# Kernel optimization log

Measured on AMD Instinct MI355X. Metric: run time of the kernel, lower is better.

Reference implementation:

```python
import jax, jax.numpy as jnp
import numpy as np

D, H, WIN, OUT = 3, 64, 8, 32
B, T = 128, 129
IU, JU = np.triu_indices(D, k=1)  # Lyndon pairs i<j at depth 2


def setup_inputs() -> dict:
    key = jax.random.key(0)
    ks = jax.random.split(key, 10)
    ts = jnp.broadcast_to(jnp.linspace(0.0, 1.0, T), (B, T))
    # path-like control values: cumulative sum of small increments
    x = jnp.cumsum(0.1 * jax.random.normal(ks[0], (B, T, D)), axis=1)
    def lin(k, o, i):
        return jax.random.normal(k, (o, i), dtype=jnp.float32) * (1.0 / np.sqrt(i))
    return {
        "ts": ts, "x": x,
        "W0": lin(ks[1], 128, D), "b0": jnp.zeros((128,), jnp.float32),
        "W1": lin(ks[2], 128, 128), "b1": jnp.zeros((128,), jnp.float32),
        "W2": lin(ks[3], H, 128), "b2": jnp.zeros((H,), jnp.float32),
        "V0": lin(ks[4], 128, H), "c0": jnp.zeros((128,), jnp.float32),
        "V1": lin(ks[5], 128, 128), "c1": jnp.zeros((128,), jnp.float32),
        "V2": lin(ks[6], D * H, 128), "c2": jnp.zeros((D * H,), jnp.float32),
        "R": lin(ks[7], OUT, H), "rb": jnp.zeros((OUT,), jnp.float32),
    }


def reference(ts, x, W0, b0, W1, b1, W2, b2, V0, c0, V1, c1, V2, c2, R, rb):
    sp = jax.nn.softplus

    def init_mlp(v):  # R^D -> R^H, Euclidean retract = identity
        return W2 @ sp(W1 @ sp(W0 @ v + b0) + b1) + b2

    def vf_flat(y):  # R^H -> R^{D*H}, final tanh (split_multi_vector_field)
        return jnp.tanh(V2 @ sp(V1 @ sp(V0 @ y + c0) + c1) + c2)

    def F(y):
        # level-1 fields f_i(y) as rows of m: (D, H)
        m = vf_flat(y).reshape(D, H)
        # J[a, b] = D f_b(y) . f_a(y)  via JVPs in directions f_a
        J = jax.vmap(lambda v: jax.jvp(vf_flat, (y,), (v,))[1].reshape(D, H))(m)
        # Lyndon level-2 brackets [f_i, f_j] = Df_j.f_i - Df_i.f_j
        br = J[IU, JU] - J[JU, IU]  # (D*(D-1)/2, H)
        return jnp.concatenate([m, br], axis=0).T  # (H, logsig_size)

    def logsigs_fn(xs):  # depth-2 log-signatures over disjoint windows
        nw = (T - 1) // WIN
        idx = (np.arange(nw) * WIN)[:, None] + np.arange(WIN + 1)[None, :]
        win = xs[idx]
        lvl1 = win[:, -1] - win[:, 0]       # increments
        rel = win[:, :-1] - win[:, :1]      # path relative to window start
        dv = win[:, 1:] - win[:, :-1]       # increments within window
        a = jnp.einsum('nki,nkj->nij', rel, dv)
        area = 0.5 * (a - jnp.swapaxes(a, 1, 2))  # Levy areas
        return jnp.concatenate([lvl1, area[:, IU, JU]], axis=1)

    def solve_one(t, xs):
        h0 = init_mlp(xs[0])
        ls = logsigs_fn(xs)                       # (nw, L)
        t_sig = t[::WIN]                          # window knot times
        slopes = ls / (t_sig[1:] - t_sig[:-1])[:, None]  # dz/dt per window
        slope_steps = jnp.repeat(slopes, WIN, axis=0)    # (T-1, L)
        dts = t[1:] - t[:-1]

        def step(y, inp):  # Heun integration of dy = F(y) dz/dt dt
            dt, s = inp
            k1 = F(y) @ s
            k2 = F(y + dt * k1) @ s
            yn = y + 0.5 * dt * (k1 + k2)
            return yn, yn

        _, ys = jax.lax.scan(step, h0, (dts, slope_steps))
        hidden = jnp.concatenate([h0[None], ys], axis=0)  # (T, H)
        return jnp.tanh(hidden @ R.T + rb)                # evolving readout

    return jax.vmap(solve_one)(ts, x)  # (B, T, OUT)
```

## Files before the change

### kernel.cpp

```cpp
#include <hip/hip_runtime.h>
#include <math.h>

#define BB 128
#define TT 129
#define NSTEP 128
#define NW 16
#define WINW 8
#define OUTD 32

typedef _Float16 h2_t __attribute__((ext_vector_type(2)));

__device__ __forceinline__ float fast_rcp(float v){ return __builtin_amdgcn_rcpf(v); }
__device__ __forceinline__ float softplus_f(float v){ return fmaxf(v,0.f)+__logf(1.f+__expf(-fabsf(v))); }
__device__ __forceinline__ float sigmoid_f(float v){ return fast_rcp(1.f+__expf(-v)); }
__device__ __forceinline__ float tanh_f(float v){
    float ax=fminf(fabsf(v),15.f); float e=__expf(2.f*ax);
    float r=1.f-2.f*fast_rcp(e+1.f); return copysignf(r,v);
}
__device__ __forceinline__ float pack2(float a,float b){
    h2_t h; h.x=(_Float16)a; h.y=(_Float16)b; return __builtin_bit_cast(float,h);
}
__device__ __forceinline__ float dot2c(float wc,float ac,float acc){
    return __builtin_amdgcn_fdot2(__builtin_bit_cast(h2_t,wc),__builtin_bit_cast(h2_t,ac),acc,false);
}
__device__ __forceinline__ float dot2q(float4 wq,float4 aq,float acc){
    acc=dot2c(wq.x,aq.x,acc); acc=dot2c(wq.y,aq.y,acc);
    acc=dot2c(wq.z,aq.z,acc); acc=dot2c(wq.w,aq.w,acc); return acc;
}
#define DOT4(acc,Wv,Av) acc += (Wv).x*(Av).x + (Wv).y*(Av).y + (Wv).z*(Av).z + (Wv).w*(Av).w
#define PIN4(v) asm volatile("" : "+v"((v).x), "+v"((v).y), "+v"((v).z), "+v"((v).w))

#define DPPF(x,ctrl) __builtin_bit_cast(float, __builtin_amdgcn_update_dpp(0, __builtin_bit_cast(int,(x)), (ctrl), 0xF, 0xF, true))
__device__ __forceinline__ float dpp_xor1(float x){ return DPPF(x,0xB1); }
__device__ __forceinline__ float dpp_xor2(float x){ return DPPF(x,0x4E); }
__device__ __forceinline__ float dpp_hmir(float x){ return DPPF(x,0x141); }

__global__ __launch_bounds__(256, 1)
void ncde_solve(const float* __restrict__ ts, const float* __restrict__ x,
                const float* __restrict__ W0, const float* __restrict__ b0,
                const float* __restrict__ W1, const float* __restrict__ b1,
                const float* __restrict__ W2, const float* __restrict__ b2,
                const float* __restrict__ V0, const float* __restrict__ c0,
                const float* __restrict__ V1, const float* __restrict__ c1,
                const float* __restrict__ V2, const float* __restrict__ c2,
                const float* __restrict__ R, const float* __restrict__ rb,
                float* __restrict__ out)
{
    const int b = blockIdx.x;
    const int tid = threadIdx.x;
    const int r = tid >> 2, q = tid & 3;
    const int prow = tid >> 3, poct = tid & 7;

    __shared__ __align__(16) float RSh[OUTD*68];
    __shared__ __align__(16) float ySh[64];
    __shared__ __align__(16) float yp[32], y2p[32];
    __shared__ __align__(16) float a0H[64], a1H[64];
    __shared__ __align__(16) float mpH[96];
    __shared__ __align__(16) float u0H[192], u1H[192];
    __shared__ float slopesSh[NW][6];
    __shared__ float dtsSh[NSTEP];

    float4 v0c[2][2], v1c[2][4], v2c[3][4];
    {
        auto pkld = [](const float* src)->float4{
            const float4* p=(const float4*)src;
            float4 a=p[0], c=p[1];
            float4 rr; rr.x=pack2(a.x,a.y); rr.y=pack2(a.z,a.w); rr.z=pack2(c.x,c.y); rr.w=pack2(c.z,c.w);
            return rr;
        };
        #pragma unroll
        for (int i=0;i<2;i++){
            const float* base = V0 + (r+64*i)*64 + q*16;
            v0c[i][0]=pkld(base); v0c[i][1]=pkld(base+8);
        }
        #pragma unroll
        for (int i=0;i<2;i++){
            const float* base = V1 + (r+64*i)*128 + q*32;
            #pragma unroll
            for (int k=0;k<4;k++) v1c[i][k]=pkld(base+8*k);
        }
        #pragma unroll
        for (int i=0;i<3;i++){
            const float* base = V2 + (r+64*i)*128 + q*32;
            #pragma unroll
            for (int k=0;k<4;k++) v2c[i][k]=pkld(base+8*k);
        }
        #pragma unroll
        for (int i=0;i<2;i++){ PIN4(v0c[i][0]); PIN4(v0c[i][1]); }
        #pragma unroll
        for (int i=0;i<2;i++){
            #pragma unroll
            for (int k=0;k<4;k++) PIN4(v1c[i][k]);
        }
        #pragma unroll
        for (int i=0;i<3;i++){
            #pragma unroll
            for (int k=0;k<4;k++) PIN4(v2c[i][k]);
        }
    }
    const float c0A=c0[r], c0B=c0[64+r];
    const float c1A=c1[r], c1B=c1[64+r];
    const float c2A=c2[r], c2B=c2[64+r], c2C=c2[128+r];
    const float rbp = rb[prow];

    for (int i=tid; i<OUTD*64; i+=256) RSh[(i>>6)*68 + (i&63)] = R[i];
    const float* tsb = ts + b*TT;
    for (int i=tid; i<NSTEP; i+=256) dtsSh[i] = tsb[i+1] - tsb[i];

    if (tid < NW) {
        const int w = tid;
        const float* xs = x + (size_t)(b*TT + w*WINW)*3;
        float x0c[3] = {xs[0], xs[1], xs[2]};
        float prev[3] = {x0c[0], x0c[1], x0c[2]};
        float am01=0.f, am02=0.f, am12=0.f, am10=0.f, am20=0.f, am21=0.f;
        #pragma unroll
        for (int k=0;k<WINW;k++) {
            float cur[3] = {xs[(k+1)*3+0], xs[(k+1)*3+1], xs[(k+1)*3+2]};
            float rel[3], dv[3];
            #pragma unroll
            for (int c=0;c<3;c++){ rel[c]=prev[c]-x0c[c]; dv[c]=cur[c]-prev[c]; }
            am01 += rel[0]*dv[1]; am10 += rel[1]*dv[0];
            am02 += rel[0]*dv[2]; am20 += rel[2]*dv[0];
            am12 += rel[1]*dv[2]; am21 += rel[2]*dv[1];
            prev[0]=cur[0]; prev[1]=cur[1]; prev[2]=cur[2];
        }
        const float invden = 1.f/(tsb[(w+1)*WINW] - tsb[w*WINW]);
        slopesSh[w][0] = (prev[0]-x0c[0])*invden;
        slopesSh[w][1] = (prev[1]-x0c[1])*invden;
        slopesSh[w][2] = (prev[2]-x0c[2])*invden;
        slopesSh[w][3] = 0.5f*(am01-am10)*invden;
        slopesSh[w][4] = 0.5f*(am02-am20)*invden;
        slopesSh[w][5] = 0.5f*(am12-am21)*invden;
    }

    if (tid < 128) {
        const float xv0 = x[(size_t)b*TT*3+0];
        const float xv1 = x[(size_t)b*TT*3+1];
        const float xv2 = x[(size_t)b*TT*3+2];
        float acc = b0[tid] + W0[tid*3]*xv0 + W0[tid*3+1]*xv1 + W0[tid*3+2]*xv2;
        u0H[tid] = softplus_f(acc);
    }
    __syncthreads();
    if (tid < 128) {
        float acc = b1[tid];
        const float4* rw = (const float4*)(W1 + tid*128);
        #pragma unroll 8
        for (int k=0;k<32;k++){ float4 wv=rw[k]; float4 av=*(const float4*)&u0H[4*k]; DOT4(acc,wv,av); }
        u1H[tid] = softplus_f(acc);
    }
    __syncthreads();
    if (tid < 64) {
        float acc = b2[tid];
        const float4* rw = (const float4*)(W2 + tid*128);
        #pragma unroll 8
        for (int k=0;k<32;k++){ float4 wv=rw[k]; float4 av=*(const float4*)&u1H[4*k]; DOT4(acc,wv,av); }
        ySh[tid] = acc;
        ((_Float16*)yp)[tid] = (_Float16)acc;
    }
    __syncthreads();

    float yreg = ySh[r];
    float k1r = 0.f;
    float S0,S1,S2,S3,S4,S5;

    auto Feval = [&](const float* ypIn, bool first, float dtc) {
        float sig0A,sig0B,sig1A,sig1B,mA,mB,mC,dtA,dtB,dtC;
        {
            const float4* Y = (const float4*)ypIn + q*2;
            float4 y0=Y[0], y1=Y[1];
            float zA=0.f, zB=0.f;
            zA=dot2q(v0c[0][0],y0,zA); zA=dot2q(v0c[0][1],y1,zA);
            zB=dot2q(v0c[1][0],y0,zB); zB=dot2q(v0c[1][1],y1,zB);
            zA += dpp_xor1(zA); zA += dpp_xor2(zA); zA += c0A;
            zB += dpp_xor1(zB); zB += dpp_xor2(zB); zB += c0B;
            sig0A=sigmoid_f(zA); sig0B=sigmoid_f(zB);
            if (!q){
                ((_Float16*)a0H)[r]    = (_Float16)softplus_f(zA);
                ((_Float16*)a0H)[64+r] = (_Float16)softplus_f(zB);
            }
        }
        __syncthreads();
        {
            const float4* A = (const float4*)a0H + q*4;
            float4 a0=A[0],a1=A[1],a2=A[2],a3=A[3];
            float zA=0.f, zB=0.f;
            zA=dot2q(v1c[0][0],a0,zA); zA=dot2q(v1c[0][1],a1,zA); zA=dot2q(v1c[0][2],a2,zA); zA=dot2q(v1c[0][3],a3,zA);
            zB=dot2q(v1c[1][0],a0,zB); zB=dot2q(v1c[1][1],a1,zB); zB=dot2q(v1c[1][2],a2,zB); zB=dot2q(v1c[1][3],a3,zB);
            zA += dpp_xor1(zA); zA += dpp_xor2(zA); zA += c1A;
            zB += dpp_xor1(zB); zB += dpp_xor2(zB); zB += c1B;
            sig1A=sigmoid_f(zA); sig1B=sigmoid_f(zB);
            if (!q){
                ((_Float16*)a1H)[r]    = (_Float16)softplus_f(zA);
                ((_Float16*)a1H)[64+r] = (_Float16)softplus_f(zB);
            }
        }
        __syncthreads();
        {
            const float4* A = (const float4*)a1H + q*4;
            float4 a0=A[0],a1=A[1],a2=A[2],a3=A[3];
            float zA=0.f, zB=0.f, zC=0.f;
            zA=dot2q(v2c[0][0],a0,zA); zA=dot2q(v2c[0][1],a1,zA); zA=dot2q(v2c[0][2],a2,zA); zA=dot2q(v2c[0][3],a3,zA);
            zB=dot2q(v2c[1][0],a0,zB); zB=dot2q(v2c[1][1],a1,zB); zB=dot2q(v2c[1][2],a2,zB); zB=dot2q(v2c[1][3],a3,zB);
            zC=dot2q(v2c[2][0],a0,zC); zC=dot2q(v2c[2][1],a1,zC); zC=dot2q(v2c[2][2],a2,zC); zC=dot2q(v2c[2][3],a3,zC);
            zA += dpp_xor1(zA); zA += dpp_xor2(zA);
            zB += dpp_xor1(zB); zB += dpp_xor2(zB);
            zC += dpp_xor1(zC); zC += dpp_xor2(zC);
            mA=tanh_f(zA+c2A); mB=tanh_f(zB+c2B); mC=tanh_f(zC+c2C);
            dtA=1.f-mA*mA; dtB=1.f-mB*mB; dtC=1.f-mC*mC;
            if (!q){
                ((_Float16*)mpH)[r]     = (_Float16)mA;
                ((_Float16*)mpH)[64+r]  = (_Float16)mB;
                ((_Float16*)mpH)[128+r] = (_Float16)mC;
            }
        }
        __syncthreads();
        {
            const float4* M = (const float4*)mpH;
            float4 g00=M[q*2], g01=M[q*2+1];
            float4 g10=M[8+q*2], g11=M[8+q*2+1];
            float4 g20=M[16+q*2], g21=M[16+q*2+1];
            float t0A=0.f,t1A=0.f,t2A=0.f,t0B=0.f,t1B=0.f,t2B=0.f;
            t0A=dot2q(v0c[0][0],g00,t0A); t0A=dot2q(v0c[0][1],g01,t0A);
            t1A=dot2q(v0c[0][0],g10,t1A); t1A=dot2q(v0c[0][1],g11,t1A);
            t2A=dot2q(v0c[0][0],g20,t2A); t2A=dot2q(v0c[0][1],g21,t2A);
            t0B=dot2q(v0c[1][0],g00,t0B); t0B=dot2q(v0c[1][1],g01,t0B);
            t1B=dot2q(v0c[1][0],g10,t1B); t1B=dot2q(v0c[1][1],g11,t1B);
            t2B=dot2q(v0c[1][0],g20,t2B); t2B=dot2q(v0c[1][1],g21,t2B);
            t0A += dpp_xor1(t0A); t0A += dpp_xor2(t0A);
            t1A += dpp_xor1(t1A); t1A += dpp_xor2(t1A);
            t2A += dpp_xor1(t2A); t2A += dpp_xor2(t2A);
            t0B += dpp_xor1(t0B); t0B += dpp_xor2(t0B);
            t1B += dpp_xor1(t1B); t1B += dpp_xor2(t1B);
            t2B += dpp_xor1(t2B); t2B += dpp_xor2(t2B);
            if (!q){
                ((_Float16*)u0H)[r]      = (_Float16)(sig0A*t0A);
                ((_Float16*)u0H)[64+r]   = (_Float16)(sig0B*t0B);
                ((_Float16*)u0H)[128+r]  = (_Float16)(sig0A*t1A);
                ((_Float16*)u0H)[192+r]  = (_Float16)(sig0B*t1B);
                ((_Float16*)u0H)[256+r]  = (_Float16)(sig0A*t2A);
                ((_Float16*)u0H)[320+r]  = (_Float16)(sig0B*t2B);
            }
        }
        __syncthreads();
        {
            const float4* U = (const float4*)u0H;
            float4 g0[4],g1[4],g2[4];
            #pragma unroll
            for (int k=0;k<4;k++){ g0[k]=U[q*4+k]; g1[k]=U[16+q*4+k]; g2[k]=U[32+q*4+k]; }
            float t0A=0.f,t1A=0.f,t2A=0.f,t0B=0.f,t1B=0.f,t2B=0.f;
            #pragma unroll
            for (int k=0;k<4;k++){
                float4 wa=v1c[0][k], wb=v1c[1][k];
                t0A=dot2q(wa,g0[k],t0A); t1A=dot2q(wa,g1[k],t1A); t2A=dot2q(wa,g2[k],t2A);
                t0B=dot2q(wb,g0[k],t0B); t1B=dot2q(wb,g1[k],t1B); t2B=dot2q(wb,g2[k],t2B);
            }
            t0A += dpp_xor1(t0A); t0A += dpp_xor2(t0A);
            t1A += dpp_xor1(t1A); t1A += dpp_xor2(t1A);
            t2A += dpp_xor1(t2A); t2A += dpp_xor2(t2A);
            t0B += dpp_xor1(t0B); t0B += dpp_xor2(t0B);
            t1B += dpp_xor1(t1B); t1B += dpp_xor2(t1B);
            t2B += dpp_xor1(t2B); t2B += dpp_xor2(t2B);
            if (!q){
                ((_Float16*)u1H)[r]      = (_Float16)(sig1A*t0A);
                ((_Float16*)u1H)[64+r]   = (_Float16)(sig1B*t0B);
                ((_Float16*)u1H)[128+r]  = (_Float16)(sig1A*t1A);
                ((_Float16*)u1H)[192+r]  = (_Float16)(sig1B*t1B);
                ((_Float16*)u1H)[256+r]  = (_Float16)(sig1A*t2A);
                ((_Float16*)u1H)[320+r]  = (_Float16)(sig1B*t2B);
            }
        }
        __syncthreads();
        {
            const float4* U = (const float4*)u1H;
            float4 g0[4],g1[4],g2[4];
            #pragma unroll
            for (int k=0;k<4;k++){ g0[k]=U[q*4+k]; g1[k]=U[16+q*4+k]; g2[k]=U[32+q*4+k]; }
            float J1r=0.f,J2r=0.f,J0m=0.f,J2m=0.f,J0t=0.f,J1t=0.f;
            #pragma unroll
            for (int k=0;k<4;k++){
                float4 wa=v2c[0][k], wb=v2c[1][k], wc=v2c[2][k];
                J1r=dot2q(wa,g1[k],J1r); J2r=dot2q(wa,g2[k],J2r);
                J0m=dot2q(wb,g0[k],J0m); J2m=dot2q(wb,g2[k],J2m);
                J0t=dot2q(wc,g0[k],J0t); J1t=dot2q(wc,g1[k],J1t);
            }
            J1r += dpp_xor1(J1r); J1r += dpp_xor2(J1r);
            J2r += dpp_xor1(J2r); J2r += dpp_xor2(J2r);
            J0m += dpp_xor1(J0m); J0m += dpp_xor2(J0m);
            J2m += dpp_xor1(J2m); J2m += dpp_xor2(J2m);
            J0t += dpp_xor1(J0t); J0t += dpp_xor2(J0t);
            J1t += dpp_xor1(J1t); J1t += dpp_xor2(J1t);
            J1r*=dtA; J2r*=dtA; J0m*=dtB; J2m*=dtB; J0t*=dtC; J1t*=dtC;
            float kk = mA*S0 + mB*S1 + mC*S2
                     + S3*(J0m - J1r) + S4*(J0t - J2r) + S5*(J1t - J2m);
            if (first){
                k1r = kk;
                float y2 = yreg + dtc*kk;
                if (!q) ((_Float16*)y2p)[r] = (_Float16)y2;
            } else {
                yreg += 0.5f*dtc*(k1r + kk);
                if (!q){ ((_Float16*)yp)[r] = (_Float16)yreg; ySh[r] = yreg; }
            }
        }
        __syncthreads();
    };

    auto proj = [&](int stp) {
        const float4* rr = (const float4*)(RSh + prow*68 + poct*8);
        const float4* yy = (const float4*)(ySh + poct*8);
        float pacc = 0.f;
        DOT4(pacc, rr[0], yy[0]); DOT4(pacc, rr[1], yy[1]);
        pacc += dpp_xor1(pacc);
        pacc += dpp_xor2(pacc);
        pacc += dpp_hmir(pacc);
        if (!poct) out[(size_t)(b*TT + stp)*OUTD + prow] = tanh_f(pacc + rbp);
    };

    for (int step=0; step<NSTEP; ++step) {
        proj(step);
        const int w = step >> 3;
        S0=slopesSh[w][0]; S1=slopesSh[w][1]; S2=slopesSh[w][2];
        S3=slopesSh[w][3]; S4=slopesSh[w][4]; S5=slopesSh[w][5];
        const float dtc = dtsSh[step];
        Feval(yp,  true,  dtc);
        Feval(y2p, false, dtc);
    }
    proj(NSTEP);
}

extern "C" void kernel_launch(void* const* d_in, const int* in_sizes, int n_in,
                              void* d_out, int out_size, void* d_ws, size_t ws_size,
                              hipStream_t stream) {
    const float* ts = (const float*)d_in[0];
    const float* x  = (const float*)d_in[1];
    const float* W0 = (const float*)d_in[2];
    const float* b0 = (const float*)d_in[3];
    const float* W1 = (const float*)d_in[4];
    const float* b1 = (const float*)d_in[5];
    const float* W2 = (const float*)d_in[6];
    const float* b2 = (const float*)d_in[7];
    const float* V0 = (const float*)d_in[8];
    const float* c0 = (const float*)d_in[9];
    const float* V1 = (const float*)d_in[10];
    const float* c1 = (const float*)d_in[11];
    const float* V2 = (const float*)d_in[12];
    const float* c2 = (const float*)d_in[13];
    const float* R  = (const float*)d_in[14];
    const float* rb = (const float*)d_in[15];
    float* out = (float*)d_out;

    ncde_solve<<<dim3(BB), dim3(256), 0, stream>>>(
        ts, x, W0, b0, W1, b1, W2, b2, V0, c0, V1, c1, V2, c2, R, rb, out);
}
```

Measured before the change: 617.2 us.

## Pack two batch elements per 512-thread block with shared barriers

Each block now handles two batch elements. Two 256-thread halves index their own per-element shared buffers and share RSh and the __syncthreads barriers. This halves the grid from 128 to 64 blocks on a GPU with many more CUs. The intent is to interleave two independent serial chains inside one CU to hide latency, but it uses fewer CUs, the shared barriers couple both halves, and register pressure per CU goes up.

New measurement: 870.4 us. +41.0%, slower.

```diff
diff --git a/kernel.cpp b/kernel.cpp
--- a/kernel.cpp
+++ b/kernel.cpp
@@ -7,6 +7,7 @@
 #define NW 16
 #define WINW 8
 #define OUTD 32
+#define NB 2
 
 typedef _Float16 h2_t __attribute__((ext_vector_type(2)));
 
@@ -35,7 +36,7 @@
 __device__ __forceinline__ float dpp_xor2(float x){ return DPPF(x,0x4E); }
 __device__ __forceinline__ float dpp_hmir(float x){ return DPPF(x,0x141); }
 
-__global__ __launch_bounds__(256, 1)
+__global__ __launch_bounds__(512, 1)
 void ncde_solve(const float* __restrict__ ts, const float* __restrict__ x,
                 const float* __restrict__ W0, const float* __restrict__ b0,
                 const float* __restrict__ W1, const float* __restrict__ b1,
@@ -46,19 +47,21 @@
                 const float* __restrict__ R, const float* __restrict__ rb,
                 float* __restrict__ out)
 {
-    const int b = blockIdx.x;
     const int tid = threadIdx.x;
-    const int r = tid >> 2, q = tid & 3;
-    const int prow = tid >> 3, poct = tid & 7;
+    const int u = tid >> 8;
+    const int t = tid & 255;
+    const int b = blockIdx.x * NB + u;
+    const int r = t >> 2, q = t & 3;
+    const int prow = t >> 3, poct = t & 7;
 
     __shared__ __align__(16) float RSh[OUTD*68];
-    __shared__ __align__(16) float ySh[64];
-    __shared__ __align__(16) float yp[32], y2p[32];
-    __shared__ __align__(16) float a0H[64], a1H[64];
-    __shared__ __align__(16) float mpH[96];
-    __shared__ __align__(16) float u0H[192], u1H[192];
-    __shared__ float slopesSh[NW][6];
-    __shared__ float dtsSh[NSTEP];
+    __shared__ __align__(16) float ySh[NB][64];
+    __shared__ __align__(16) float yp[NB][32], y2p[NB][32];
+    __shared__ __align__(16) float a0H[NB][64], a1H[NB][64];
+    __shared__ __align__(16) float mpH[NB][96];
+    __shared__ __align__(16) float u0H[NB][192], u1H[NB][192];
+    __shared__ float slopesSh[NB][NW][6];
+    __shared__ float dtsSh[NB][NSTEP];
 
     float4 v0c[2][2], v1c[2][4], v2c[3][4];
     {
@@ -103,12 +106,12 @@
     const float c2A=c2[r], c2B=c2[64+r], c2C=c2[128+r];
     const float rbp = rb[prow];
 
-    for (int i=tid; i<OUTD*64; i+=256) RSh[(i>>6)*68 + (i&63)] = R[i];
-    const float* tsb = ts + b*TT;
-    for (int i=tid; i<NSTEP; i+=256) dtsSh[i] = tsb[i+1] - tsb[i];
-
-    if (tid < NW) {
-        const int w = tid;
+    for (int i=tid; i<OUTD*64; i+=512) RSh[(i>>6)*68 + (i&63)] = R[i];
+    const float* tsb = ts + (size_t)b*TT;
+    for (int i=t; i<NSTEP; i+=256) dtsSh[u][i] = tsb[i+1] - tsb[i];
+
+    if (t < NW) {
+        const int w = t;
         const float* xs = x + (size_t)(b*TT + w*WINW)*3;
         float x0c[3] = {xs[0], xs[1], xs[2]};
         float prev[3] = {x0c[0], x0c[1], x0c[2]};
@@ -125,41 +128,41 @@
             prev[0]=cur[0]; prev[1]=cur[1]; prev[2]=cur[2];
         }
         const float invden = 1.f/(tsb[(w+1)*WINW] - tsb[w*WINW]);
-        slopesSh[w][0] = (prev[0]-x0c[0])*invden;
-        slopesSh[w][1] = (prev[1]-x0c[1])*invden;
-        slopesSh[w][2] = (prev[2]-x0c[2])*invden;
-        slopesSh[w][3] = 0.5f*(am01-am10)*invden;
-        slopesSh[w][4] = 0.5f*(am02-am20)*invden;
-        slopesSh[w][5] = 0.5f*(am12-am21)*invden;
-    }
-
-    if (tid < 128) {
+        slopesSh[u][w][0] = (prev[0]-x0c[0])*invden;
+        slopesSh[u][w][1] = (prev[1]-x0c[1])*invden;
+        slopesSh[u][w][2] = (prev[2]-x0c[2])*invden;
+        slopesSh[u][w][3] = 0.5f*(am01-am10)*invden;
+        slopesSh[u][w][4] = 0.5f*(am02-am20)*invden;
+        slopesSh[u][w][5] = 0.5f*(am12-am21)*invden;
+    }
+
+    if (t < 128) {
         const float xv0 = x[(size_t)b*TT*3+0];
         const float xv1 = x[(size_t)b*TT*3+1];
         const float xv2 = x[(size_t)b*TT*3+2];
-        float acc = b0[tid] + W0[tid*3]*xv0 + W0[tid*3+1]*xv1 + W0[tid*3+2]*xv2;
-        u0H[tid] = softplus_f(acc);
+        float acc = b0[t] + W0[t*3]*xv0 + W0[t*3+1]*xv1 + W0[t*3+2]*xv2;
+        u0H[u][t] = softplus_f(acc);
     }
     __syncthreads();
-    if (tid < 128) {
-        float acc = b1[tid];
-        const float4* rw = (const float4*)(W1 + tid*128);
+    if (t < 128) {
+        float acc = b1[t];
+        const float4* rw = (const float4*)(W1 + t*128);
         #pragma unroll 8
-        for (int k=0;k<32;k++){ float4 wv=rw[k]; float4 av=*(const float4*)&u0H[4*k]; DOT4(acc,wv,av); }
-        u1H[tid] = softplus_f(acc);
+        for (int k=0;k<32;k++){ float4 wv=rw[k]; float4 av=*(const float4*)&u0H[u][4*k]; DOT4(acc,wv,av); }
+        u1H[u][t] = softplus_f(acc);
     }
     __syncthreads();
-    if (tid < 64) {
-        float acc = b2[tid];
-        const float4* rw = (const float4*)(W2 + tid*128);
+    if (t < 64) {
+        float acc = b2[t];
+        const float4* rw = (const float4*)(W2 + t*128);
         #pragma unroll 8
-        for (int k=0;k<32;k++){ float4 wv=rw[k]; float4 av=*(const float4*)&u1H[4*k]; DOT4(acc,wv,av); }
-        ySh[tid] = acc;
-        ((_Float16*)yp)[tid] = (_Float16)acc;
+        for (int k=0;k<32;k++){ float4 wv=rw[k]; float4 av=*(const float4*)&u1H[u][4*k]; DOT4(acc,wv,av); }
+        ySh[u][t] = acc;
+        ((_Float16*)yp[u])[t] = (_Float16)acc;
     }
     __syncthreads();
 
-    float yreg = ySh[r];
+    float yreg = ySh[u][r];
     float k1r = 0.f;
     float S0,S1,S2,S3,S4,S5;
 
@@ -175,13 +178,13 @@
             zB += dpp_xor1(zB); zB += dpp_xor2(zB); zB += c0B;
             sig0A=sigmoid_f(zA); sig0B=sigmoid_f(zB);
             if (!q){
-                ((_Float16*)a0H)[r]    = (_Float16)softplus_f(zA);
-                ((_Float16*)a0H)[64+r] = (_Float16)softplus_f(zB);
-            }
-        }
-        __syncthreads();
-        {
-            const float4* A = (const float4*)a0H + q*4;
+                ((_Float16*)a0H[u])[r]    = (_Float16)softplus_f(zA);
+                ((_Float16*)a0H[u])[64+r] = (_Float16)softplus_f(zB);
+            }
+        }
+        __syncthreads();
+        {
+            const float4* A = (const float4*)a0H[u] + q*4;
             float4 a0=A[0],a1=A[1],a2=A[2],a3=A[3];
             float zA=0.f, zB=0.f;
             zA=dot2q(v1c[0][0],a0,zA); zA=dot2q(v1c[0][1],a1,zA); zA=dot2q(v1c[0][2],a2,zA); zA=dot2q(v1c[0][3],a3,zA);
@@ -190,13 +193,13 @@
             zB += dpp_xor1(zB); zB += dpp_xor2(zB); zB += c1B;
             sig1A=sigmoid_f(zA); sig1B=sigmoid_f(zB);
             if (!q){
-                ((_Float16*)a1H)[r]    = (_Float16)softplus_f(zA);
-                ((_Float16*)a1H)[64+r] = (_Float16)softplus_f(zB);
-            }
-        }
-        __syncthreads();
-        {
-            const float4* A = (const float4*)a1H + q*4;
+                ((_Float16*)a1H[u])[r]    = (_Float16)softplus_f(zA);
+                ((_Float16*)a1H[u])[64+r] = (_Float16)softplus_f(zB);
+            }
+        }
+        __syncthreads();
+        {
+            const float4* A = (const float4*)a1H[u] + q*4;
             float4 a0=A[0],a1=A[1],a2=A[2],a3=A[3];
             float zA=0.f, zB=0.f, zC=0.f;
             zA=dot2q(v2c[0][0],a0,zA); zA=dot2q(v2c[0][1],a1,zA); zA=dot2q(v2c[0][2],a2,zA); zA=dot2q(v2c[0][3],a3,zA);
@@ -208,14 +211,14 @@
             mA=tanh_f(zA+c2A); mB=tanh_f(zB+c2B); mC=tanh_f(zC+c2C);
             dtA=1.f-mA*mA; dtB=1.f-mB*mB; dtC=1.f-mC*mC;
             if (!q){
-                ((_Float16*)mpH)[r]     = (_Float16)mA;
-                ((_Float16*)mpH)[64+r]  = (_Float16)mB;
-                ((_Float16*)mpH)[128+r] = (_Float16)mC;
-            }
-        }
-        __syncthreads();
-        {
-            const float4* M = (const float4*)mpH;
+                ((_Float16*)mpH[u])[r]     = (_Float16)mA;
+                ((_Float16*)mpH[u])[64+r]  = (_Float16)mB;
+                ((_Float16*)mpH[u])[128+r] = (_Float16)mC;
+            }
+        }
+        __syncthreads();
+        {
+            const float4* M = (const float4*)mpH[u];
             float4 g00=M[q*2], g01=M[q*2+1];
             float4 g10=M[8+q*2], g11=M[8+q*2+1];
             float4 g20=M[16+q*2], g21=M[16+q*2+1];
@@ -233,17 +236,17 @@
             t1B += dpp_xor1(t1B); t1B += dpp_xor2(t1B);
             t2B += dpp_xor1(t2B); t2B += dpp_xor2(t2B);
             if (!q){
-                ((_Float16*)u0H)[r]      = (_Float16)(sig0A*t0A);
-                ((_Float16*)u0H)[64+r]   = (_Float16)(sig0B*t0B);
-                ((_Float16*)u0H)[128+r]  = (_Float16)(sig0A*t1A);
-                ((_Float16*)u0H)[192+r]  = (_Float16)(sig0B*t1B);
-                ((_Float16*)u0H)[256+r]  = (_Float16)(sig0A*t2A);
-                ((_Float16*)u0H)[320+r]  = (_Float16)(sig0B*t2B);
-            }
-        }
-        __syncthreads();
-        {
-            const float4* U = (const float4*)u0H;
+                ((_Float16*)u0H[u])[r]      = (_Float16)(sig0A*t0A);
+                ((_Float16*)u0H[u])[64+r]   = (_Float16)(sig0B*t0B);
+                ((_Float16*)u0H[u])[128+r]  = (_Float16)(sig0A*t1A);
+                ((_Float16*)u0H[u])[192+r]  = (_Float16)(sig0B*t1B);
+                ((_Float16*)u0H[u])[256+r]  = (_Float16)(sig0A*t2A);
+                ((_Float16*)u0H[u])[320+r]  = (_Float16)(sig0B*t2B);
+            }
+        }
+        __syncthreads();
+        {
+            const float4* U = (const float4*)u0H[u];
             float4 g0[4],g1[4],g2[4];
             #pragma unroll
             for (int k=0;k<4;k++){ g0[k]=U[q*4+k]; g1[k]=U[16+q*4+k]; g2[k]=U[32+q*4+k]; }
@@ -261,17 +264,17 @@
             t1B += dpp_xor1(t1B); t1B += dpp_xor2(t1B);
             t2B += dpp_xor1(t2B); t2B += dpp_xor2(t2B);
             if (!q){
-                ((_Float16*)u1H)[r]      = (_Float16)(sig1A*t0A);
-                ((_Float16*)u1H)[64+r]   = (_Float16)(sig1B*t0B);
-                ((_Float16*)u1H)[128+r]  = (_Float16)(sig1A*t1A);
-                ((_Float16*)u1H)[192+r]  = (_Float16)(sig1B*t1B);
-                ((_Float16*)u1H)[256+r]  = (_Float16)(sig1A*t2A);
-                ((_Float16*)u1H)[320+r]  = (_Float16)(sig1B*t2B);
-            }
-        }
-        __syncthreads();
-        {
-            const float4* U = (const float4*)u1H;
+                ((_Float16*)u1H[u])[r]      = (_Float16)(sig1A*t0A);
+                ((_Float16*)u1H[u])[64+r]   = (_Float16)(sig1B*t0B);
+                ((_Float16*)u1H[u])[128+r]  = (_Float16)(sig1A*t1A);
+                ((_Float16*)u1H[u])[192+r]  = (_Float16)(sig1B*t1B);
+                ((_Float16*)u1H[u])[256+r]  = (_Float16)(sig1A*t2A);
+                ((_Float16*)u1H[u])[320+r]  = (_Float16)(sig1B*t2B);
+            }
+        }
+        __syncthreads();
+        {
+            const float4* U = (const float4*)u1H[u];
             float4 g0[4],g1[4],g2[4];
             #pragma unroll
             for (int k=0;k<4;k++){ g0[k]=U[q*4+k]; g1[k]=U[16+q*4+k]; g2[k]=U[32+q*4+k]; }
@@ -295,10 +298,10 @@
             if (first){
                 k1r = kk;
                 float y2 = yreg + dtc*kk;
-                if (!q) ((_Float16*)y2p)[r] = (_Float16)y2;
+                if (!q) ((_Float16*)y2p[u])[r] = (_Float16)y2;
             } else {
                 yreg += 0.5f*dtc*(k1r + kk);
-                if (!q){ ((_Float16*)yp)[r] = (_Float16)yreg; ySh[r] = yreg; }
+                if (!q){ ((_Float16*)yp[u])[r] = (_Float16)yreg; ySh[u][r] = yreg; }
             }
         }
         __syncthreads();
@@ -306,7 +309,7 @@
 
     auto proj = [&](int stp) {
         const float4* rr = (const float4*)(RSh + prow*68 + poct*8);
-        const float4* yy = (const float4*)(ySh + poct*8);
+        const float4* yy = (const float4*)(ySh[u] + poct*8);
         float pacc = 0.f;
         DOT4(pacc, rr[0], yy[0]); DOT4(pacc, rr[1], yy[1]);
         pacc += dpp_xor1(pacc);
@@ -318,11 +321,11 @@
     for (int step=0; step<NSTEP; ++step) {
         proj(step);
         const int w = step >> 3;
-        S0=slopesSh[w][0]; S1=slopesSh[w][1]; S2=slopesSh[w][2];
-        S3=slopesSh[w][3]; S4=slopesSh[w][4]; S5=slopesSh[w][5];
-        const float dtc = dtsSh[step];
-        Feval(yp,  true,  dtc);
-        Feval(y2p, false, dtc);
+        S0=slopesSh[u][w][0]; S1=slopesSh[u][w][1]; S2=slopesSh[u][w][2];
+        S3=slopesSh[u][w][3]; S4=slopesSh[u][w][4]; S5=slopesSh[u][w][5];
+        const float dtc = dtsSh[u][step];
+        Feval(yp[u],  true,  dtc);
+        Feval(y2p[u], false, dtc);
     }
     proj(NSTEP);
 }
@@ -348,6 +351,6 @@
     const float* rb = (const float*)d_in[15];
     float* out = (float*)d_out;
 
-    ncde_solve<<<dim3(BB), dim3(256), 0, stream>>>(
+    ncde_solve<<<dim3(BB/NB), dim3(512), 0, stream>>>(
         ts, x, W0, b0, W1, b1, W2, b2, V0, c0, V1, c1, V2, c2, R, rb, out);
 }
```

## Split each row's dot products across eight lanes with 512-thread blocks

Applied to the files above, without the earlier changes.

Doubles the block size to 512 threads and assigns each output row to 8 lanes instead of 4. Each lane now keeps half as many packed fp16 weights in registers and performs half as many dot2 ops per stage, with a three-step DPP reduction replacing the two-step one. The intent is to shorten the serial per-step critical path of the latency-bound Heun loop. The cost is more waves taking part in every barrier and one extra cross-lane reduction step per dot product.

New measurement: 692.0 us. 12.1% more time.

```diff
diff --git a/kernel.cpp b/kernel.cpp
--- a/kernel.cpp
+++ b/kernel.cpp
@@ -34,8 +34,9 @@
 __device__ __forceinline__ float dpp_xor1(float x){ return DPPF(x,0xB1); }
 __device__ __forceinline__ float dpp_xor2(float x){ return DPPF(x,0x4E); }
 __device__ __forceinline__ float dpp_hmir(float x){ return DPPF(x,0x141); }
-
-__global__ __launch_bounds__(256, 1)
+#define RED8(x) do{ x += dpp_xor1(x); x += dpp_xor2(x); x += dpp_hmir(x); }while(0)
+
+__global__ __launch_bounds__(512, 1)
 void ncde_solve(const float* __restrict__ ts, const float* __restrict__ x,
                 const float* __restrict__ W0, const float* __restrict__ b0,
                 const float* __restrict__ W1, const float* __restrict__ b1,
@@ -47,9 +48,9 @@
                 float* __restrict__ out)
 {
     const int b = blockIdx.x;
-    const int tid = threadIdx.x;
-    const int r = tid >> 2, q = tid & 3;
-    const int prow = tid >> 3, poct = tid & 7;
+    const int t = threadIdx.x;
+    const int r = t >> 3, q = t & 7;
+    const int prow = t >> 3, poct = t & 7;
 
     __shared__ __align__(16) float RSh[OUTD*68];
     __shared__ __align__(16) float ySh[64];
@@ -60,7 +61,7 @@
     __shared__ float slopesSh[NW][6];
     __shared__ float dtsSh[NSTEP];
 
-    float4 v0c[2][2], v1c[2][4], v2c[3][4];
+    float4 v0c[2], v1c[2][2], v2c[3][2];
     {
         auto pkld = [](const float* src)->float4{
             const float4* p=(const float4*)src;
@@ -69,46 +70,35 @@
             return rr;
         };
         #pragma unroll
+        for (int i=0;i<2;i++) v0c[i]=pkld(V0 + (r+64*i)*64 + q*8);
+        #pragma unroll
         for (int i=0;i<2;i++){
-            const float* base = V0 + (r+64*i)*64 + q*16;
-            v0c[i][0]=pkld(base); v0c[i][1]=pkld(base+8);
-        }
-        #pragma unroll
-        for (int i=0;i<2;i++){
-            const float* base = V1 + (r+64*i)*128 + q*32;
-            #pragma unroll
-            for (int k=0;k<4;k++) v1c[i][k]=pkld(base+8*k);
+            const float* base = V1 + (r+64*i)*128 + q*16;
+            v1c[i][0]=pkld(base); v1c[i][1]=pkld(base+8);
         }
         #pragma unroll
         for (int i=0;i<3;i++){
-            const float* base = V2 + (r+64*i)*128 + q*32;
-            #pragma unroll
-            for (int k=0;k<4;k++) v2c[i][k]=pkld(base+8*k);
-        }
-        #pragma unroll
-        for (int i=0;i<2;i++){ PIN4(v0c[i][0]); PIN4(v0c[i][1]); }
-        #pragma unroll
-        for (int i=0;i<2;i++){
-            #pragma unroll
-            for (int k=0;k<4;k++) PIN4(v1c[i][k]);
-        }
-        #pragma unroll
-        for (int i=0;i<3;i++){
-            #pragma unroll
-            for (int k=0;k<4;k++) PIN4(v2c[i][k]);
-        }
+            const float* base = V2 + (r+64*i)*128 + q*16;
+            v2c[i][0]=pkld(base); v2c[i][1]=pkld(base+8);
+        }
+        #pragma unroll
+        for (int i=0;i<2;i++) PIN4(v0c[i]);
+        #pragma unroll
+        for (int i=0;i<2;i++){ PIN4(v1c[i][0]); PIN4(v1c[i][1]); }
+        #pragma unroll
+        for (int i=0;i<3;i++){ PIN4(v2c[i][0]); PIN4(v2c[i][1]); }
     }
     const float c0A=c0[r], c0B=c0[64+r];
     const float c1A=c1[r], c1B=c1[64+r];
     const float c2A=c2[r], c2B=c2[64+r], c2C=c2[128+r];
-    const float rbp = rb[prow];
-
-    for (int i=tid; i<OUTD*64; i+=256) RSh[(i>>6)*68 + (i&63)] = R[i];
-    const float* tsb = ts + b*TT;
-    for (int i=tid; i<NSTEP; i+=256) dtsSh[i] = tsb[i+1] - tsb[i];
-
-    if (tid < NW) {
-        const int w = tid;
+    const float rbp = rb[prow & 31];
+
+    for (int i=t; i<OUTD*64; i+=512) RSh[(i>>6)*68 + (i&63)] = R[i];
+    const float* tsb = ts + (size_t)b*TT;
+    if (t < NSTEP) dtsSh[t] = tsb[t+1] - tsb[t];
+
+    if (t < NW) {
+        const int w = t;
         const float* xs = x + (size_t)(b*TT + w*WINW)*3;
         float x0c[3] = {xs[0], xs[1], xs[2]};
         float prev[3] = {x0c[0], x0c[1], x0c[2]};
@@ -133,29 +123,29 @@
         slopesSh[w][5] = 0.5f*(am12-am21)*invden;
     }
 
-    if (tid < 128) {
+    if (t < 128) {
         const float xv0 = x[(size_t)b*TT*3+0];
         const float xv1 = x[(size_t)b*TT*3+1];
         const float xv2 = x[(size_t)b*TT*3+2];
-        float acc = b0[tid] + W0[tid*3]*xv0 + W0[tid*3+1]*xv1 + W0[tid*3+2]*xv2;
-        u0H[tid] = softplus_f(acc);
+        float acc = b0[t] + W0[t*3]*xv0 + W0[t*3+1]*xv1 + W0[t*3+2]*xv2;
+        u0H[t] = softplus_f(acc);
     }
     __syncthreads();
-    if (tid < 128) {
-        float acc = b1[tid];
-        const float4* rw = (const float4*)(W1 + tid*128);
+    if (t < 128) {
+        float acc = b1[t];
+        const float4* rw = (const float4*)(W1 + t*128);
         #pragma unroll 8
         for (int k=0;k<32;k++){ float4 wv=rw[k]; float4 av=*(const float4*)&u0H[4*k]; DOT4(acc,wv,av); }
-        u1H[tid] = softplus_f(acc);
+        u1H[t] = softplus_f(acc);
     }
     __syncthreads();
-    if (tid < 64) {
-        float acc = b2[tid];
-        const float4* rw = (const float4*)(W2 + tid*128);
+    if (t < 64) {
+        float acc = b2[t];
+        const float4* rw = (const float4*)(W2 + t*128);
         #pragma unroll 8
         for (int k=0;k<32;k++){ float4 wv=rw[k]; float4 av=*(const float4*)&u1H[4*k]; DOT4(acc,wv,av); }
-        ySh[tid] = acc;
-        ((_Float16*)yp)[tid] = (_Float16)acc;
+        ySh[t] = acc;
+        ((_Float16*)yp)[t] = (_Float16)acc;
     }
     __syncthreads();
 
@@ -166,13 +156,11 @@
     auto Feval = [&](const float* ypIn, bool first, float dtc) {
         float sig0A,sig0B,sig1A,sig1B,mA,mB,mC,dtA,dtB,dtC;
         {
-            const float4* Y = (const float4*)ypIn + q*2;
-            float4 y0=Y[0], y1=Y[1];
-            float zA=0.f, zB=0.f;
-            zA=dot2q(v0c[0][0],y0,zA); zA=dot2q(v0c[0][1],y1,zA);
-            zB=dot2q(v0c[1][0],y0,zB); zB=dot2q(v0c[1][1],y1,zB);
-            zA += dpp_xor1(zA); zA += dpp_xor2(zA); zA += c0A;
-            zB += dpp_xor1(zB); zB += dpp_xor2(zB); zB += c0B;
+            float4 y0 = ((const float4*)ypIn)[q];
+            float zA=dot2q(v0c[0],y0,0.f);
+            float zB=dot2q(v0c[1],y0,0.f);
+            RED8(zA); RED8(zB);
+            zA += c0A; zB += c0B;
             sig0A=sigmoid_f(zA); sig0B=sigmoid_f(zB);
             if (!q){
                 ((_Float16*)a0H)[r]    = (_Float16)softplus_f(zA);
@@ -181,13 +169,12 @@
         }
         __syncthreads();
         {
-            const float4* A = (const float4*)a0H + q*4;
-            float4 a0=A[0],a1=A[1],a2=A[2],a3=A[3];
-            float zA=0.f, zB=0.f;
-            zA=dot2q(v1c[0][0],a0,zA); zA=dot2q(v1c[0][1],a1,zA); zA=dot2q(v1c[0][2],a2,zA); zA=dot2q(v1c[0][3],a3,zA);
-            zB=dot2q(v1c[1][0],a0,zB); zB=dot2q(v1c[1][1],a1,zB); zB=dot2q(v1c[1][2],a2,zB); zB=dot2q(v1c[1][3],a3,zB);
-            zA += dpp_xor1(zA); zA += dpp_xor2(zA); zA += c1A;
-            zB += dpp_xor1(zB); zB += dpp_xor2(zB); zB += c1B;
+            const float4* A = (const float4*)a0H + q*2;
+            float4 a0=A[0], a1=A[1];
+            float zA=dot2q(v1c[0][0],a0,0.f); zA=dot2q(v1c[0][1],a1,zA);
+            float zB=dot2q(v1c[1][0],a0,0.f); zB=dot2q(v1c[1][1],a1,zB);
+            RED8(zA); RED8(zB);
+            zA += c1A; zB += c1B;
             sig1A=sigmoid_f(zA); sig1B=sigmoid_f(zB);
             if (!q){
                 ((_Float16*)a1H)[r]    = (_Float16)softplus_f(zA);
@@ -196,15 +183,12 @@
         }
         __syncthreads();
         {
-            const float4* A = (const float4*)a1H + q*4;
-            float4 a0=A[0],a1=A[1],a2=A[2],a3=A[3];
-            float zA=0.f, zB=0.f, zC=0.f;
-            zA=dot2q(v2c[0][0],a0,zA); zA=dot2q(v2c[0][1],a1,zA); zA=dot2q(v2c[0][2],a2,zA); zA=dot2q(v2c[0][3],a3,zA);
-            zB=dot2q(v2c[1][0],a0,zB); zB=dot2q(v2c[1][1],a1,zB); zB=dot2q(v2c[1][2],a2,zB); zB=dot2q(v2c[1][3],a3,zB);
-            zC=dot2q(v2c[2][0],a0,zC); zC=dot2q(v2c[2][1],a1,zC); zC=dot2q(v2c[2][2],a2,zC); zC=dot2q(v2c[2][3],a3,zC);
-            zA += dpp_xor1(zA); zA += dpp_xor2(zA);
-            zB += dpp_xor1(zB); zB += dpp_xor2(zB);
-            zC += dpp_xor1(zC); zC += dpp_xor2(zC);
+            const float4* A = (const float4*)a1H + q*2;
+            float4 a0=A[0], a1=A[1];
+            float zA=dot2q(v2c[0][0],a0,0.f); zA=dot2q(v2c[0][1],a1,zA);
+            float zB=dot2q(v2c[1][0],a0,0.f); zB=dot2q(v2c[1][1],a1,zB);
+            float zC=dot2q(v2c[2][0],a0,0.f); zC=dot2q(v2c[2][1],a1,zC);
+            RED8(zA); RED8(zB); RED8(zC);
             mA=tanh_f(zA+c2A); mB=tanh_f(zB+c2B); mC=tanh_f(zC+c2C);
             dtA=1.f-mA*mA; dtB=1.f-mB*mB; dtC=1.f-mC*mC;
             if (!q){
@@ -216,22 +200,11 @@
         __syncthreads();
         {
             const float4* M = (const float4*)mpH;
-            float4 g00=M[q*2], g01=M[q*2+1];
-            float4 g10=M[8+q*2], g11=M[8+q*2+1];
-            float4 g20=M[16+q*2], g21=M[16+q*2+1];
-            float t0A=0.f,t1A=0.f,t2A=0.f,t0B=0.f,t1B=0.f,t2B=0.f;
-            t0A=dot2q(v0c[0][0],g00,t0A); t0A=dot2q(v0c[0][1],g01,t0A);
-            t1A=dot2q(v0c[0][0],g10,t1A); t1A=dot2q(v0c[0][1],g11,t1A);
-            t2A=dot2q(v0c[0][0],g20,t2A); t2A=dot2q(v0c[0][1],g21,t2A);
-            t0B=dot2q(v0c[1][0],g00,t0B); t0B=dot2q(v0c[1][1],g01,t0B);
-            t1B=dot2q(v0c[1][0],g10,t1B); t1B=dot2q(v0c[1][1],g11,t1B);
-            t2B=dot2q(v0c[1][0],g20,t2B); t2B=dot2q(v0c[1][1],g21,t2B);
-            t0A += dpp_xor1(t0A); t0A += dpp_xor2(t0A);
-            t1A += dpp_xor1(t1A); t1A += dpp_xor2(t1A);
-            t2A += dpp_xor1(t2A); t2A += dpp_xor2(t2A);
-            t0B += dpp_xor1(t0B); t0B += dpp_xor2(t0B);
-            t1B += dpp_xor1(t1B); t1B += dpp_xor2(t1B);
-            t2B += dpp_xor1(t2B); t2B += dpp_xor2(t2B);
+            float4 g0=M[q], g1=M[8+q], g2=M[16+q];
+            float t0A=dot2q(v0c[0],g0,0.f), t1A=dot2q(v0c[0],g1,0.f), t2A=dot2q(v0c[0],g2,0.f);
+            float t0B=dot2q(v0c[1],g0,0.f), t1B=dot2q(v0c[1],g1,0.f), t2B=dot2q(v0c[1],g2,0.f);
+            RED8(t0A); RED8(t1A); RED8(t2A);
+            RED8(t0B); RED8(t1B); RED8(t2B);
             if (!q){
                 ((_Float16*)u0H)[r]      = (_Float16)(sig0A*t0A);
                 ((_Float16*)u0H)[64+r]   = (_Float16)(sig0B*t0B);
@@ -244,22 +217,17 @@
         __syncthreads();
         {
             const float4* U = (const float4*)u0H;
-            float4 g0[4],g1[4],g2[4];
-            #pragma unroll
-            for (int k=0;k<4;k++){ g0[k]=U[q*4+k]; g1[k]=U[16+q*4+k]; g2[k]=U[32+q*4+k]; }
-            float t0A=0.f,t1A=0.f,t2A=0.f,t0B=0.f,t1B=0.f,t2B=0.f;
-            #pragma unroll
-            for (int k=0;k<4;k++){
-                float4 wa=v1c[0][k], wb=v1c[1][k];
-                t0A=dot2q(wa,g0[k],t0A); t1A=dot2q(wa,g1[k],t1A); t2A=dot2q(wa,g2[k],t2A);
-                t0B=dot2q(wb,g0[k],t0B); t1B=dot2q(wb,g1[k],t1B); t2B=dot2q(wb,g2[k],t2B);
-            }
-            t0A += dpp_xor1(t0A); t0A += dpp_xor2(t0A);
-            t1A += dpp_xor1(t1A); t1A += dpp_xor2(t1A);
-            t2A += dpp_xor1(t2A); t2A += dpp_xor2(t2A);
-            t0B += dpp_xor1(t0B); t0B += dpp_xor2(t0B);
-            t1B += dpp_xor1(t1B); t1B += dpp_xor2(t1B);
-            t2B += dpp_xor1(t2B); t2B += dpp_xor2(t2B);
+            float4 g0a=U[q*2],    g0b=U[q*2+1];
+            float4 g1a=U[16+q*2], g1b=U[16+q*2+1];
+            float4 g2a=U[32+q*2], g2b=U[32+q*2+1];
+            float t0A=dot2q(v1c[0][0],g0a,0.f); t0A=dot2q(v1c[0][1],g0b,t0A);
+            float t1A=dot2q(v1c[0][0],g1a,0.f); t1A=dot2q(v1c[0][1],g1b,t1A);
+            float t2A=dot2q(v1c[0][0],g2a,0.f); t2A=dot2q(v1c[0][1],g2b,t2A);
+            float t0B=dot2q(v1c[1][0],g0a,0.f); t0B=dot2q(v1c[1][1],g0b,t0B);
+            float t1B=dot2q(v1c[1][0],g1a,0.f); t1B=dot2q(v1c[1][1],g1b,t1B);
+            float t2B=dot2q(v1c[1][0],g2a,0.f); t2B=dot2q(v1c[1][1],g2b,t2B);
+            RED8(t0A); RED8(t1A); RED8(t2A);
+            RED8(t0B); RED8(t1B); RED8(t2B);
             if (!q){
                 ((_Float16*)u1H)[r]      = (_Float16)(sig1A*t0A);
                 ((_Float16*)u1H)[64+r]   = (_Float16)(sig1B*t0B);
@@ -272,23 +240,16 @@
         __syncthreads();
         {
             const float4* U = (const float4*)u1H;
-            float4 g0[4],g1[4],g2[4];
-            #pragma unroll
-            for (int k=0;k<4;k++){ g0[k]=U[q*4+k]; g1[k]=U[16+q*4+k]; g2[k]=U[32+q*4+k]; }
-            float J1r=0.f,J2r=0.f,J0m=0.f,J2m=0.f,J0t=0.f,J1t=0.f;
-            #pragma unroll
-            for (int k=0;k<4;k++){
-                float4 wa=v2c[0][k], wb=v2c[1][k], wc=v2c[2][k];
-                J1r=dot2q(wa,g1[k],J1r); J2r=dot2q(wa,g2[k],J2r);
-                J0m=dot2q(wb,g0[k],J0m); J2m=dot2q(wb,g2[k],J2m);
-                J0t=dot2q(wc,g0[k],J0t); J1t=dot2q(wc,g1[k],J1t);
-            }
-            J1r += dpp_xor1(J1r); J1r += dpp_xor2(J1r);
-            J2r += dpp_xor1(J2r); J2r += dpp_xor2(J2r);
-            J0m += dpp_xor1(J0m); J0m += dpp_xor2(J0m);
-            J2m += dpp_xor1(J2m); J2m += dpp_xor2(J2m);
-            J0t += dpp_xor1(J0t); J0t += dpp_xor2(J0t);
-            J1t += dpp_xor1(J1t); J1t += dpp_xor2(J1t);
+            float4 g0a=U[q*2],    g0b=U[q*2+1];
+            float4 g1a=U[16+q*2], g1b=U[16+q*2+1];
+            float4 g2a=U[32+q*2], g2b=U[32+q*2+1];
+            float J1r=dot2q(v2c[0][0],g1a,0.f); J1r=dot2q(v2c[0][1],g1b,J1r);
+            float J2r=dot2q(v2c[0][0],g2a,0.f); J2r=dot2q(v2c[0][1],g2b,J2r);
+            float J0m=dot2q(v2c[1][0],g0a,0.f); J0m=dot2q(v2c[1][1],g0b,J0m);
+            float J2m=dot2q(v2c[1][0],g2a,0.f); J2m=dot2q(v2c[1][1],g2b,J2m);
+            float J0t=dot2q(v2c[2][0],g0a,0.f); J0t=dot2q(v2c[2][1],g0b,J0t);
+            float J1t=dot2q(v2c[2][0],g1a,0.f); J1t=dot2q(v2c[2][1],g1b,J1t);
+            RED8(J1r); RED8(J2r); RED8(J0m); RED8(J2m); RED8(J0t); RED8(J1t);
             J1r*=dtA; J2r*=dtA; J0m*=dtB; J2m*=dtB; J0t*=dtC; J1t*=dtC;
             float kk = mA*S0 + mB*S1 + mC*S2
                      + S3*(J0m - J1r) + S4*(J0t - J2r) + S5*(J1t - J2m);
@@ -305,14 +266,16 @@
     };
 
     auto proj = [&](int stp) {
-        const float4* rr = (const float4*)(RSh + prow*68 + poct*8);
-        const float4* yy = (const float4*)(ySh + poct*8);
-        float pacc = 0.f;
-        DOT4(pacc, rr[0], yy[0]); DOT4(pacc, rr[1], yy[1]);
-        pacc += dpp_xor1(pacc);
-        pacc += dpp_xor2(pacc);
-        pacc += dpp_hmir(pacc);
-        if (!poct) out[(size_t)(b*TT + stp)*OUTD + prow] = tanh_f(pacc + rbp);
+        if (t < 256){
+            const float4* rr = (const float4*)(RSh + prow*68 + poct*8);
+            const float4* yy = (const float4*)(ySh + poct*8);
+            float pacc = 0.f;
+            DOT4(pacc, rr[0], yy[0]); DOT4(pacc, rr[1], yy[1]);
+            pacc += dpp_xor1(pacc);
+            pacc += dpp_xor2(pacc);
+            pacc += dpp_hmir(pacc);
+            if (!poct) out[(size_t)(b*TT + stp)*OUTD + prow] = tanh_f(pacc + rbp);
+        }
     };
 
     for (int step=0; step<NSTEP; ++step) {
@@ -348,6 +311,6 @@
     const float* rb = (const float*)d_in[15];
     float* out = (float*)d_out;
 
-    ncde_solve<<<dim3(BB), dim3(256), 0, stream>>>(
+    ncde_solve<<<dim3(BB), dim3(512), 0, stream>>>(
         ts, x, W0, b0, W1, b1, W2, b2, V0, c0, V1, c1, V2, c2, R, rb, out);
 }
```
